# Optimization experiments

Hardware: AMD Instinct MI355X
Metric: run time of the kernel (lower is better)

## Reference

```python
import jax, jax.numpy as jnp
import numpy as np

RCUT = 6.0
EPS = 1e-6
NUM_BASIS = 8
P = 6  # PolynomialSmooth envelope power
N_NODES = 100000
N_EDGES = 3200000
N_GRAPHS = 16

# 27 periodic image shifts: all integer combos of [-1,0,1]^3
_PERIODIC = jnp.asarray(
    np.stack(np.meshgrid(*([[-1, 0, 1]] * 3), indexing='ij'), -1).reshape(27, 3).astype(np.float32)
)


def _sh_lmax2(u):
    """e3nn spherical harmonics, lmax=2, normalize=True, normalization='component'.
    u: [E,3] unit vectors -> [E,9]."""
    x, y, z = u[..., 0], u[..., 1], u[..., 2]
    s3 = jnp.sqrt(jnp.asarray(3.0, u.dtype))
    s5 = jnp.sqrt(jnp.asarray(5.0, u.dtype))
    s15 = jnp.sqrt(jnp.asarray(15.0, u.dtype))
    return jnp.stack([
        jnp.ones_like(x),                      # l=0
        s3 * x, s3 * y, s3 * z,                # l=1
        s15 * x * z,                           # l=2
        s15 * x * y,
        s5 * (y * y - 0.5 * (x * x + z * z)),
        s15 * y * z,
        0.5 * s15 * (z * z - x * x),
    ], axis=-1)


def _bessel(lengths):
    # lengths: [E,1] -> [E,NUM_BASIS]
    k = jnp.arange(1, NUM_BASIS + 1, dtype=lengths.dtype) * jnp.pi / RCUT
    safe = jnp.clip(lengths, EPS, RCUT)
    return jnp.sin(safe * k) / (2.0 * safe)


def _poly_smooth(lengths):
    # standard polynomial envelope (DimeNet-style), zero at r=rcut
    x = jnp.clip(lengths / RCUT, 0.0, 1.0)
    c1 = (P + 1) * (P + 2) / 2.0
    c2 = float(P * (P + 2))
    c3 = P * (P + 1) / 2.0
    xp = x ** P
    return 1.0 - c1 * xp + c2 * xp * x - c3 * xp * x * x


def setup_inputs() -> dict:
    key = jax.random.key(0)
    k1, k2, k3, k4, k5 = jax.random.split(key, 5)
    pos = jax.random.normal(k1, (N_NODES, 3), dtype=jnp.float32) * 5.0
    cells = jax.random.normal(k2, (N_GRAPHS, 3, 3), dtype=jnp.float32)
    edge_index = jax.random.randint(k3, (2, N_EDGES), 0, N_NODES)
    periodic_index = jax.random.randint(k4, (N_EDGES,), 0, 27)
    batch = jnp.sort(jax.random.randint(k5, (N_NODES,), 0, N_GRAPHS))
    return {"pos": pos, "cells": cells, "edge_index": edge_index,
            "periodic_index": periodic_index, "batch": batch}


def reference(pos, cells, edge_index, periodic_index, batch):
    node_src, node_dst = edge_index[0], edge_index[1]
    vectors = pos[node_dst] - pos[node_src]                     # [E,3]
    shifts = _PERIODIC[periodic_index]                          # [E,3]
    src_cells = cells[batch[node_src]]                          # [E,3,3]
    vectors = vectors - jnp.einsum('eij,ei->ej', src_cells, shifts)
    vectors = -vectors                                          # dst == 'atom'
    lengths = jnp.linalg.norm(vectors, axis=-1, keepdims=True)  # [E,1]
    unit = vectors / jnp.maximum(lengths, EPS)                  # normalize=True
    attr = _sh_lmax2(unit)                                      # [E,9]
    basis = _bessel(lengths)                                    # [E,8]
    cutoff = _poly_smooth(lengths)                              # [E,1]
    basis_weight = basis * cutoff                               # [E,8]
    # pack (length, sh attr, smooth, basis_weight) -> [E,19]
    return jnp.concatenate([lengths, attr, cutoff, basis_weight], axis=-1)
```

## Files before the change

kernel.cpp:

```cpp
#include <hip/hip_runtime.h>

#define BLOCK 256

typedef float vf4 __attribute__((ext_vector_type(4)));

extern "C" __global__ void __launch_bounds__(BLOCK) pack_pos_batch(
    const float* __restrict__ pos,
    const int*  __restrict__ batch,
    vf4* __restrict__ pos4,
    int N)
{
    const int i = blockIdx.x * BLOCK + threadIdx.x;
    if (i < N) {
        vf4 v;
        v.x = pos[3 * i + 0];
        v.y = pos[3 * i + 1];
        v.z = pos[3 * i + 2];
        v.w = __int_as_float(batch[i]);
        pos4[i] = v;
    }
}

template <bool PACKED>
__global__ void __launch_bounds__(BLOCK) edge_encoding_kernel(
    const float* __restrict__ pos,
    const vf4*   __restrict__ pos4,
    const float* __restrict__ cells,
    const int*   __restrict__ eidx,
    const int*   __restrict__ pidx,
    const int*   __restrict__ batch,
    float* __restrict__ out,
    int E)
{
    __shared__ float s_cells[144];
    __shared__ __align__(16) float s_out[BLOCK * 19];

    const int tid = threadIdx.x;
    if (tid < 144) s_cells[tid] = cells[tid];
    __syncthreads();

    const int base = blockIdx.x * BLOCK;
    const int e = base + tid;

    float row[19];
    if (e < E) {
        const int src = __builtin_nontemporal_load(eidx + e);
        const int dst = __builtin_nontemporal_load(eidx + E + e);
        const int p   = __builtin_nontemporal_load(pidx + e);

        float sx, sy, sz, dx, dy, dz;
        int g;
        if (PACKED) {
            const vf4 ps = pos4[src];
            const vf4 pd = pos4[dst];
            sx = ps.x; sy = ps.y; sz = ps.z;
            dx = pd.x; dy = pd.y; dz = pd.z;
            g  = __float_as_int(ps.w);
        } else {
            sx = pos[3*src+0]; sy = pos[3*src+1]; sz = pos[3*src+2];
            dx = pos[3*dst+0]; dy = pos[3*dst+1]; dz = pos[3*dst+2];
            g  = batch[src];
        }

        const float f0 = (float)(p / 9 - 1);
        const float f1 = (float)((p / 3) % 3 - 1);
        const float f2 = (float)(p % 3 - 1);

        const float* C = s_cells + g * 9;
        const float tx = C[0]*f0 + C[3]*f1 + C[6]*f2;
        const float ty = C[1]*f0 + C[4]*f1 + C[7]*f2;
        const float tz = C[2]*f0 + C[5]*f1 + C[8]*f2;

        const float vx = sx - dx + tx;
        const float vy = sy - dy + ty;
        const float vz = sz - dz + tz;

        const float len  = sqrtf(vx*vx + vy*vy + vz*vz);
        const float invl = 1.0f / fmaxf(len, 1e-6f);
        const float x = vx * invl, y = vy * invl, z = vz * invl;

        const float s3  = 1.7320508075688772f;
        const float s5  = 2.2360679774997896f;
        const float s15 = 3.872983346207417f;

        row[0] = len;
        row[1] = 1.0f;
        row[2] = s3 * x;
        row[3] = s3 * y;
        row[4] = s3 * z;
        row[5] = s15 * x * z;
        row[6] = s15 * x * y;
        row[7] = s5  * (y*y - 0.5f*(x*x + z*z));
        row[8] = s15 * y * z;
        row[9] = 0.5f * s15 * (z*z - x*x);

        const float xc = fminf(len * (1.0f/6.0f), 1.0f);
        const float x3 = xc * xc * xc;
        const float x6 = x3 * x3;
        const float cut = fmaf(x6, fmaf(xc, fmaf(-21.0f, xc, 48.0f), -28.0f), 1.0f);
        row[10] = cut;

        const float safe = fminf(fmaxf(len, 1e-6f), 6.0f);
        const float a = safe * 0.5235987755982988f;
        const float sa = __sinf(a);
        const float ca = __cosf(a);
        const float w = cut / (2.0f * safe);
        const float two_ca = 2.0f * ca;
        float s_prev = 0.0f, s_cur = sa;
        row[11] = s_cur * w;
        #pragma unroll
        for (int n = 2; n <= 8; ++n) {
            const float s_next = two_ca * s_cur - s_prev;
            s_prev = s_cur;
            s_cur  = s_next;
            row[10 + n] = s_cur * w;
        }
    } else {
        #pragma unroll
        for (int j = 0; j < 19; ++j) row[j] = 0.0f;
    }

    #pragma unroll
    for (int j = 0; j < 19; ++j) s_out[tid * 19 + j] = row[j];
    __syncthreads();

    const int nvalid  = min(BLOCK, E - base);
    const int nfloats = nvalid * 19;
    float* gout = out + (size_t)base * 19;
    const int n4 = nfloats >> 2;
    const vf4* s4 = reinterpret_cast<const vf4*>(s_out);
    vf4* g4 = reinterpret_cast<vf4*>(gout);
    for (int i = tid; i < n4; i += BLOCK)
        __builtin_nontemporal_store(s4[i], g4 + i);
    for (int i = (n4 << 2) + tid; i < nfloats; i += BLOCK)
        __builtin_nontemporal_store(s_out[i], gout + i);
}

extern "C" void kernel_launch(void* const* d_in, const int* in_sizes, int n_in,
                              void* d_out, int out_size, void* d_ws, size_t ws_size,
                              hipStream_t stream) {
    const float* pos   = (const float*)d_in[0];
    const float* cells = (const float*)d_in[1];
    const int*   eidx  = (const int*)d_in[2];
    const int*   pidx  = (const int*)d_in[3];
    const int*   batch = (const int*)d_in[4];
    float* out = (float*)d_out;

    const int E = in_sizes[3];
    const int N = in_sizes[4];
    const int grid = (E + BLOCK - 1) / BLOCK;

    if (d_ws != nullptr && ws_size >= (size_t)N * sizeof(vf4)) {
        vf4* pos4 = (vf4*)d_ws;
        const int pgrid = (N + BLOCK - 1) / BLOCK;
        pack_pos_batch<<<pgrid, BLOCK, 0, stream>>>(pos, batch, pos4, N);
        edge_encoding_kernel<true><<<grid, BLOCK, 0, stream>>>(
            pos, pos4, cells, eidx, pidx, batch, out, E);
    } else {
        edge_encoding_kernel<false><<<grid, BLOCK, 0, stream>>>(
            pos, nullptr, cells, eidx, pidx, batch, out, E);
    }
}
```

Measured before the change: 294.6 us.

## Convert edge kernel to persistent grid with software-pipelined index loads and gathers

The edge kernel now runs on a fixed grid of 2048 persistent blocks that loop over tiles. Each iteration prefetches indices two tiles ahead and position gathers one tile ahead, and writes the previous tile's staged output while the current tile is computed. The goal is to hide gather latency and overlap output stores with compute. The two divisions are also replaced with fast hardware reciprocals. The cost is higher register pressure and extra barriers per tile, and the reciprocal is slightly less accurate.

```diff
diff --git a/kernel.cpp b/kernel.cpp
--- a/kernel.cpp
+++ b/kernel.cpp
@@ -1,6 +1,7 @@
 #include <hip/hip_runtime.h>
 
 #define BLOCK 256
+#define NBLOCKS 2048
 
 typedef float vf4 __attribute__((ext_vector_type(4)));
 
@@ -37,103 +38,149 @@
 
     const int tid = threadIdx.x;
     if (tid < 144) s_cells[tid] = cells[tid];
+
+    const int ntiles = (E + BLOCK - 1) / BLOCK;
+    const int nb = gridDim.x;
+
+    const float s3  = 1.7320508075688772f;
+    const float s5  = 2.2360679774997896f;
+    const float s15 = 3.872983346207417f;
+
+    int src1, dst1, p0, p1;
+    vf4 g_ps, g_pd;
+
+    auto load_idx = [&](int tt, int& s, int& d, int& p) {
+        if (tt < ntiles) {
+            int e = tt * BLOCK + tid;
+            e = min(e, E - 1);
+            s = __builtin_nontemporal_load(eidx + e);
+            d = __builtin_nontemporal_load(eidx + E + e);
+            p = __builtin_nontemporal_load(pidx + e);
+        } else { s = 0; d = 0; p = 13; }
+    };
+    auto gather = [&](int s, int d, vf4& a, vf4& b) {
+        if (PACKED) {
+            a = pos4[s];
+            b = pos4[d];
+        } else {
+            a.x = pos[3*s+0]; a.y = pos[3*s+1]; a.z = pos[3*s+2];
+            a.w = __int_as_float(batch[s]);
+            b.x = pos[3*d+0]; b.y = pos[3*d+1]; b.z = pos[3*d+2];
+            b.w = 0.0f;
+        }
+    };
+
+    int t = blockIdx.x;
+    {
+        int s0, d0;
+        load_idx(t, s0, d0, p0);
+        gather(s0, d0, g_ps, g_pd);
+        load_idx(t + nb, src1, dst1, p1);
+    }
     __syncthreads();
 
-    const int base = blockIdx.x * BLOCK;
-    const int e = base + tid;
-
-    float row[19];
-    if (e < E) {
-        const int src = __builtin_nontemporal_load(eidx + e);
-        const int dst = __builtin_nontemporal_load(eidx + E + e);
-        const int p   = __builtin_nontemporal_load(pidx + e);
-
-        float sx, sy, sz, dx, dy, dz;
-        int g;
-        if (PACKED) {
-            const vf4 ps = pos4[src];
-            const vf4 pd = pos4[dst];
-            sx = ps.x; sy = ps.y; sz = ps.z;
-            dx = pd.x; dy = pd.y; dz = pd.z;
-            g  = __float_as_int(ps.w);
-        } else {
-            sx = pos[3*src+0]; sy = pos[3*src+1]; sz = pos[3*src+2];
-            dx = pos[3*dst+0]; dy = pos[3*dst+1]; dz = pos[3*dst+2];
-            g  = batch[src];
+    int tprev = -1;
+    for (; t < ntiles; t += nb) {
+        int src2, dst2, p2;
+        load_idx(t + 2 * nb, src2, dst2, p2);
+        vf4 n_ps, n_pd;
+        gather(src1, dst1, n_ps, n_pd);
+
+        if (tprev >= 0) {
+            const int nvalid  = min(BLOCK, E - tprev * BLOCK);
+            const int nfloats = nvalid * 19;
+            float* gout = out + (size_t)tprev * BLOCK * 19;
+            const int n4 = nfloats >> 2;
+            const vf4* s4 = reinterpret_cast<const vf4*>(s_out);
+            vf4* g4 = reinterpret_cast<vf4*>(gout);
+            for (int i = tid; i < n4; i += BLOCK)
+                __builtin_nontemporal_store(s4[i], g4 + i);
+            for (int i = (n4 << 2) + tid; i < nfloats; i += BLOCK)
+                __builtin_nontemporal_store(s_out[i], gout + i);
         }
 
-        const float f0 = (float)(p / 9 - 1);
-        const float f1 = (float)((p / 3) % 3 - 1);
-        const float f2 = (float)(p % 3 - 1);
-
-        const float* C = s_cells + g * 9;
-        const float tx = C[0]*f0 + C[3]*f1 + C[6]*f2;
-        const float ty = C[1]*f0 + C[4]*f1 + C[7]*f2;
-        const float tz = C[2]*f0 + C[5]*f1 + C[8]*f2;
-
-        const float vx = sx - dx + tx;
-        const float vy = sy - dy + ty;
-        const float vz = sz - dz + tz;
-
-        const float len  = sqrtf(vx*vx + vy*vy + vz*vz);
-        const float invl = 1.0f / fmaxf(len, 1e-6f);
-        const float x = vx * invl, y = vy * invl, z = vz * invl;
-
-        const float s3  = 1.7320508075688772f;
-        const float s5  = 2.2360679774997896f;
-        const float s15 = 3.872983346207417f;
-
-        row[0] = len;
-        row[1] = 1.0f;
-        row[2] = s3 * x;
-        row[3] = s3 * y;
-        row[4] = s3 * z;
-        row[5] = s15 * x * z;
-        row[6] = s15 * x * y;
-        row[7] = s5  * (y*y - 0.5f*(x*x + z*z));
-        row[8] = s15 * y * z;
-        row[9] = 0.5f * s15 * (z*z - x*x);
-
-        const float xc = fminf(len * (1.0f/6.0f), 1.0f);
-        const float x3 = xc * xc * xc;
-        const float x6 = x3 * x3;
-        const float cut = fmaf(x6, fmaf(xc, fmaf(-21.0f, xc, 48.0f), -28.0f), 1.0f);
-        row[10] = cut;
-
-        const float safe = fminf(fmaxf(len, 1e-6f), 6.0f);
-        const float a = safe * 0.5235987755982988f;
-        const float sa = __sinf(a);
-        const float ca = __cosf(a);
-        const float w = cut / (2.0f * safe);
-        const float two_ca = 2.0f * ca;
-        float s_prev = 0.0f, s_cur = sa;
-        row[11] = s_cur * w;
+        float row[19];
+        {
+            const float sx = g_ps.x, sy = g_ps.y, sz = g_ps.z;
+            const float dx = g_pd.x, dy = g_pd.y, dz = g_pd.z;
+            const int   g  = PACKED ? __float_as_int(g_ps.w)
+                                    : __float_as_int(g_ps.w);
+            const int   p  = p0;
+
+            const float f0 = (float)(p / 9 - 1);
+            const float f1 = (float)((p / 3) % 3 - 1);
+            const float f2 = (float)(p % 3 - 1);
+
+            const float* C = s_cells + g * 9;
+            const float tx = C[0]*f0 + C[3]*f1 + C[6]*f2;
+            const float ty = C[1]*f0 + C[4]*f1 + C[7]*f2;
+            const float tz = C[2]*f0 + C[5]*f1 + C[8]*f2;
+
+            const float vx = sx - dx + tx;
+            const float vy = sy - dy + ty;
+            const float vz = sz - dz + tz;
+
+            const float len  = sqrtf(vx*vx + vy*vy + vz*vz);
+            const float invl = __builtin_amdgcn_rcpf(fmaxf(len, 1e-6f));
+            const float x = vx * invl, y = vy * invl, z = vz * invl;
+
+            row[0] = len;
+            row[1] = 1.0f;
+            row[2] = s3 * x;
+            row[3] = s3 * y;
+            row[4] = s3 * z;
+            row[5] = s15 * x * z;
+            row[6] = s15 * x * y;
+            row[7] = s5  * (y*y - 0.5f*(x*x + z*z));
+            row[8] = s15 * y * z;
+            row[9] = 0.5f * s15 * (z*z - x*x);
+
+            const float xc = fminf(len * (1.0f/6.0f), 1.0f);
+            const float x3 = xc * xc * xc;
+            const float x6 = x3 * x3;
+            const float cut = fmaf(x6, fmaf(xc, fmaf(-21.0f, xc, 48.0f), -28.0f), 1.0f);
+            row[10] = cut;
+
+            const float safe = fminf(fmaxf(len, 1e-6f), 6.0f);
+            const float a = safe * 0.5235987755982988f;
+            const float sa = __sinf(a);
+            const float ca = __cosf(a);
+            const float w = cut * 0.5f * __builtin_amdgcn_rcpf(safe);
+            const float two_ca = 2.0f * ca;
+            float s_prev = 0.0f, s_cur = sa;
+            row[11] = s_cur * w;
+            #pragma unroll
+            for (int n = 2; n <= 8; ++n) {
+                const float s_next = two_ca * s_cur - s_prev;
+                s_prev = s_cur;
+                s_cur  = s_next;
+                row[10 + n] = s_cur * w;
+            }
+        }
+
+        __syncthreads();
         #pragma unroll
-        for (int n = 2; n <= 8; ++n) {
-            const float s_next = two_ca * s_cur - s_prev;
-            s_prev = s_cur;
-            s_cur  = s_next;
-            row[10 + n] = s_cur * w;
-        }
-    } else {
-        #pragma unroll
-        for (int j = 0; j < 19; ++j) row[j] = 0.0f;
-    }
-
-    #pragma unroll
-    for (int j = 0; j < 19; ++j) s_out[tid * 19 + j] = row[j];
-    __syncthreads();
-
-    const int nvalid  = min(BLOCK, E - base);
-    const int nfloats = nvalid * 19;
-    float* gout = out + (size_t)base * 19;
-    const int n4 = nfloats >> 2;
-    const vf4* s4 = reinterpret_cast<const vf4*>(s_out);
-    vf4* g4 = reinterpret_cast<vf4*>(gout);
-    for (int i = tid; i < n4; i += BLOCK)
-        __builtin_nontemporal_store(s4[i], g4 + i);
-    for (int i = (n4 << 2) + tid; i < nfloats; i += BLOCK)
-        __builtin_nontemporal_store(s_out[i], gout + i);
+        for (int j = 0; j < 19; ++j) s_out[tid * 19 + j] = row[j];
+        __syncthreads();
+
+        g_ps = n_ps; g_pd = n_pd;
+        p0 = p1;
+        src1 = src2; dst1 = dst2; p1 = p2;
+        tprev = t;
+    }
+
+    if (tprev >= 0) {
+        const int nvalid  = min(BLOCK, E - tprev * BLOCK);
+        const int nfloats = nvalid * 19;
+        float* gout = out + (size_t)tprev * BLOCK * 19;
+        const int n4 = nfloats >> 2;
+        const vf4* s4 = reinterpret_cast<const vf4*>(s_out);
+        vf4* g4 = reinterpret_cast<vf4*>(gout);
+        for (int i = tid; i < n4; i += BLOCK)
+            __builtin_nontemporal_store(s4[i], g4 + i);
+        for (int i = (n4 << 2) + tid; i < nfloats; i += BLOCK)
+            __builtin_nontemporal_store(s_out[i], gout + i);
+    }
 }
 
 extern "C" void kernel_launch(void* const* d_in, const int* in_sizes, int n_in,
@@ -148,7 +195,8 @@
 
     const int E = in_sizes[3];
     const int N = in_sizes[4];
-    const int grid = (E + BLOCK - 1) / BLOCK;
+    const int ntiles = (E + BLOCK - 1) / BLOCK;
+    const int grid = ntiles < NBLOCKS ? ntiles : NBLOCKS;
 
     if (d_ws != nullptr && ws_size >= (size_t)N * sizeof(vf4)) {
         vf4* pos4 = (vf4*)d_ws;
```

Measured after the change: 311.5 us. +5.7%, slower.

## Process four edges per thread with vector loads and direct vector stores

Applied to the files above, without the earlier changes.

Each thread now handles four consecutive edges. It loads the src, dst and periodic indices as int4 vectors and writes its 76 output floats straight to global memory as 19 float4 nontemporal stores, so the LDS staging buffer and its second barrier are gone. The 16x27 periodic translation table is precomputed into shared memory per block, and the divides are replaced with hardware reciprocal approximations. The per-thread buffer raises register pressure and may reduce occupancy. Each lane's stores are contiguous, so across a wavefront they are strided rather than fully coalesced.

```diff
diff --git a/kernel.cpp b/kernel.cpp
--- a/kernel.cpp
+++ b/kernel.cpp
@@ -1,8 +1,10 @@
 #include <hip/hip_runtime.h>
 
 #define BLOCK 256
+#define EPT 4
 
 typedef float vf4 __attribute__((ext_vector_type(4)));
+typedef int   vi4 __attribute__((ext_vector_type(4)));
 
 extern "C" __global__ void __launch_bounds__(BLOCK) pack_pos_batch(
     const float* __restrict__ pos,
@@ -32,57 +34,83 @@
     float* __restrict__ out,
     int E)
 {
-    __shared__ float s_cells[144];
-    __shared__ __align__(16) float s_out[BLOCK * 19];
+    __shared__ vf4 s_t[16 * 27];
 
     const int tid = threadIdx.x;
-    if (tid < 144) s_cells[tid] = cells[tid];
-    __syncthreads();
-
-    const int base = blockIdx.x * BLOCK;
-    const int e = base + tid;
-
-    float row[19];
-    if (e < E) {
-        const int src = __builtin_nontemporal_load(eidx + e);
-        const int dst = __builtin_nontemporal_load(eidx + E + e);
-        const int p   = __builtin_nontemporal_load(pidx + e);
-
-        float sx, sy, sz, dx, dy, dz;
-        int g;
-        if (PACKED) {
-            const vf4 ps = pos4[src];
-            const vf4 pd = pos4[dst];
-            sx = ps.x; sy = ps.y; sz = ps.z;
-            dx = pd.x; dy = pd.y; dz = pd.z;
-            g  = __float_as_int(ps.w);
-        } else {
-            sx = pos[3*src+0]; sy = pos[3*src+1]; sz = pos[3*src+2];
-            dx = pos[3*dst+0]; dy = pos[3*dst+1]; dz = pos[3*dst+2];
-            g  = batch[src];
-        }
-
+    for (int c = tid; c < 16 * 27; c += BLOCK) {
+        const int g = c / 27, p = c % 27;
         const float f0 = (float)(p / 9 - 1);
         const float f1 = (float)((p / 3) % 3 - 1);
         const float f2 = (float)(p % 3 - 1);
+        const float* C = cells + g * 9;
+        vf4 t;
+        t.x = C[0]*f0 + C[3]*f1 + C[6]*f2;
+        t.y = C[1]*f0 + C[4]*f1 + C[7]*f2;
+        t.z = C[2]*f0 + C[5]*f1 + C[8]*f2;
+        t.w = 0.0f;
+        s_t[c] = t;
+    }
+    __syncthreads();
 
-        const float* C = s_cells + g * 9;
-        const float tx = C[0]*f0 + C[3]*f1 + C[6]*f2;
-        const float ty = C[1]*f0 + C[4]*f1 + C[7]*f2;
-        const float tz = C[2]*f0 + C[5]*f1 + C[8]*f2;
+    const long long gtid = (long long)blockIdx.x * BLOCK + tid;
+    const long long e0   = gtid * EPT;
+    if (e0 >= E) return;
 
-        const float vx = sx - dx + tx;
-        const float vy = sy - dy + ty;
-        const float vz = sz - dz + tz;
+    const bool full = (e0 + EPT <= (long long)E);
+    const bool evec = ((E & 3) == 0);
+
+    int src[EPT], dst[EPT], pp[EPT];
+    if (full && evec) {
+        const vi4 s = __builtin_nontemporal_load((const vi4*)(eidx + e0));
+        const vi4 d = __builtin_nontemporal_load((const vi4*)(eidx + E + e0));
+        const vi4 q = __builtin_nontemporal_load((const vi4*)(pidx + e0));
+        src[0]=s.x; src[1]=s.y; src[2]=s.z; src[3]=s.w;
+        dst[0]=d.x; dst[1]=d.y; dst[2]=d.z; dst[3]=d.w;
+        pp[0]=q.x;  pp[1]=q.y;  pp[2]=q.z;  pp[3]=q.w;
+    } else {
+        #pragma unroll
+        for (int k = 0; k < EPT; ++k) {
+            long long e = e0 + k; if (e >= E) e = E - 1;
+            src[k] = eidx[e];
+            dst[k] = eidx[E + e];
+            pp[k]  = pidx[e];
+        }
+    }
+
+    vf4 ps[EPT], pd[EPT];
+    #pragma unroll
+    for (int k = 0; k < EPT; ++k) {
+        if (PACKED) {
+            ps[k] = pos4[src[k]];
+            pd[k] = pos4[dst[k]];
+        } else {
+            const int s = src[k], d = dst[k];
+            ps[k].x = pos[3*s+0]; ps[k].y = pos[3*s+1]; ps[k].z = pos[3*s+2];
+            ps[k].w = __int_as_float(batch[s]);
+            pd[k].x = pos[3*d+0]; pd[k].y = pos[3*d+1]; pd[k].z = pos[3*d+2];
+            pd[k].w = 0.0f;
+        }
+    }
+
+    const float s3  = 1.7320508075688772f;
+    const float s5  = 2.2360679774997896f;
+    const float s15 = 3.872983346207417f;
+
+    float buf[EPT * 19];
+    #pragma unroll
+    for (int k = 0; k < EPT; ++k) {
+        const int g = __float_as_int(ps[k].w);
+        const vf4 t = s_t[g * 27 + pp[k]];
+
+        const float vx = ps[k].x - pd[k].x + t.x;
+        const float vy = ps[k].y - pd[k].y + t.y;
+        const float vz = ps[k].z - pd[k].z + t.z;
 
         const float len  = sqrtf(vx*vx + vy*vy + vz*vz);
-        const float invl = 1.0f / fmaxf(len, 1e-6f);
+        const float invl = __builtin_amdgcn_rcpf(fmaxf(len, 1e-6f));
         const float x = vx * invl, y = vy * invl, z = vz * invl;
 
-        const float s3  = 1.7320508075688772f;
-        const float s5  = 2.2360679774997896f;
-        const float s15 = 3.872983346207417f;
-
+        float* row = buf + k * 19;
         row[0] = len;
         row[1] = 1.0f;
         row[2] = s3 * x;
@@ -104,7 +132,7 @@
         const float a = safe * 0.5235987755982988f;
         const float sa = __sinf(a);
         const float ca = __cosf(a);
-        const float w = cut / (2.0f * safe);
+        const float w = cut * 0.5f * __builtin_amdgcn_rcpf(safe);
         const float two_ca = 2.0f * ca;
         float s_prev = 0.0f, s_cur = sa;
         row[11] = s_cur * w;
@@ -115,25 +143,22 @@
             s_cur  = s_next;
             row[10 + n] = s_cur * w;
         }
-    } else {
-        #pragma unroll
-        for (int j = 0; j < 19; ++j) row[j] = 0.0f;
     }
 
-    #pragma unroll
-    for (int j = 0; j < 19; ++j) s_out[tid * 19 + j] = row[j];
-    __syncthreads();
-
-    const int nvalid  = min(BLOCK, E - base);
-    const int nfloats = nvalid * 19;
-    float* gout = out + (size_t)base * 19;
-    const int n4 = nfloats >> 2;
-    const vf4* s4 = reinterpret_cast<const vf4*>(s_out);
-    vf4* g4 = reinterpret_cast<vf4*>(gout);
-    for (int i = tid; i < n4; i += BLOCK)
-        __builtin_nontemporal_store(s4[i], g4 + i);
-    for (int i = (n4 << 2) + tid; i < nfloats; i += BLOCK)
-        __builtin_nontemporal_store(s_out[i], gout + i);
+    float* gout = out + e0 * 19;
+    if (full) {
+        #pragma unroll
+        for (int i = 0; i < 19; ++i) {
+            vf4 v;
+            v.x = buf[4*i+0]; v.y = buf[4*i+1]; v.z = buf[4*i+2]; v.w = buf[4*i+3];
+            __builtin_nontemporal_store(v, (vf4*)gout + i);
+        }
+    } else {
+        const int nvalid = (int)(E - e0);
+        for (int k = 0; k < nvalid; ++k)
+            for (int j = 0; j < 19; ++j)
+                gout[k*19 + j] = buf[k*19 + j];
+    }
 }
 
 extern "C" void kernel_launch(void* const* d_in, const int* in_sizes, int n_in,
@@ -148,7 +173,7 @@
 
     const int E = in_sizes[3];
     const int N = in_sizes[4];
-    const int grid = (E + BLOCK - 1) / BLOCK;
+    const int grid = (int)(((long long)E + BLOCK * EPT - 1) / (BLOCK * EPT));
 
     if (d_ws != nullptr && ws_size >= (size_t)N * sizeof(vf4)) {
         vf4* pos4 = (vf4*)d_ws;
```

Measured after the change: 805.7 us. 2.73x slower.

## Process four edges per thread with batched gathers and precomputed shift table

Applied to the files above, without the earlier changes.

Each thread now handles four edges, issuing all index loads and then all position gathers before computing, so more memory requests are in flight per thread. Cell-times-shift translations for all 16 graphs and 27 images are precomputed into shared memory, and the divides are replaced with hardware reciprocal approximations. The shared staging buffer is reused per sub-tile, which adds extra barriers and raises register pressure, and launches four times fewer blocks.

```diff
diff --git a/kernel.cpp b/kernel.cpp
--- a/kernel.cpp
+++ b/kernel.cpp
@@ -1,6 +1,8 @@
 #include <hip/hip_runtime.h>
 
 #define BLOCK 256
+#define EPT 4
+#define TILE (BLOCK * EPT)
 
 typedef float vf4 __attribute__((ext_vector_type(4)));
 
@@ -32,108 +34,124 @@
     float* __restrict__ out,
     int E)
 {
-    __shared__ float s_cells[144];
+    __shared__ vf4 s_t[16 * 27];
     __shared__ __align__(16) float s_out[BLOCK * 19];
 
     const int tid = threadIdx.x;
-    if (tid < 144) s_cells[tid] = cells[tid];
-    __syncthreads();
-
-    const int base = blockIdx.x * BLOCK;
-    const int e = base + tid;
-
-    float row[19];
-    if (e < E) {
-        const int src = __builtin_nontemporal_load(eidx + e);
-        const int dst = __builtin_nontemporal_load(eidx + E + e);
-        const int p   = __builtin_nontemporal_load(pidx + e);
-
-        float sx, sy, sz, dx, dy, dz;
-        int g;
-        if (PACKED) {
-            const vf4 ps = pos4[src];
-            const vf4 pd = pos4[dst];
-            sx = ps.x; sy = ps.y; sz = ps.z;
-            dx = pd.x; dy = pd.y; dz = pd.z;
-            g  = __float_as_int(ps.w);
-        } else {
-            sx = pos[3*src+0]; sy = pos[3*src+1]; sz = pos[3*src+2];
-            dx = pos[3*dst+0]; dy = pos[3*dst+1]; dz = pos[3*dst+2];
-            g  = batch[src];
-        }
-
+    for (int c = tid; c < 16 * 27; c += BLOCK) {
+        const int g = c / 27, p = c % 27;
         const float f0 = (float)(p / 9 - 1);
         const float f1 = (float)((p / 3) % 3 - 1);
         const float f2 = (float)(p % 3 - 1);
+        const float* C = cells + g * 9;
+        vf4 t;
+        t.x = C[0]*f0 + C[3]*f1 + C[6]*f2;
+        t.y = C[1]*f0 + C[4]*f1 + C[7]*f2;
+        t.z = C[2]*f0 + C[5]*f1 + C[8]*f2;
+        t.w = 0.0f;
+        s_t[c] = t;
+    }
+    __syncthreads();
 
-        const float* C = s_cells + g * 9;
-        const float tx = C[0]*f0 + C[3]*f1 + C[6]*f2;
-        const float ty = C[1]*f0 + C[4]*f1 + C[7]*f2;
-        const float tz = C[2]*f0 + C[5]*f1 + C[8]*f2;
+    const long long b0 = (long long)blockIdx.x * TILE;
 
-        const float vx = sx - dx + tx;
-        const float vy = sy - dy + ty;
-        const float vz = sz - dz + tz;
-
-        const float len  = sqrtf(vx*vx + vy*vy + vz*vz);
-        const float invl = 1.0f / fmaxf(len, 1e-6f);
-        const float x = vx * invl, y = vy * invl, z = vz * invl;
-
-        const float s3  = 1.7320508075688772f;
-        const float s5  = 2.2360679774997896f;
-        const float s15 = 3.872983346207417f;
-
-        row[0] = len;
-        row[1] = 1.0f;
-        row[2] = s3 * x;
-        row[3] = s3 * y;
-        row[4] = s3 * z;
-        row[5] = s15 * x * z;
-        row[6] = s15 * x * y;
-        row[7] = s5  * (y*y - 0.5f*(x*x + z*z));
-        row[8] = s15 * y * z;
-        row[9] = 0.5f * s15 * (z*z - x*x);
-
-        const float xc = fminf(len * (1.0f/6.0f), 1.0f);
-        const float x3 = xc * xc * xc;
-        const float x6 = x3 * x3;
-        const float cut = fmaf(x6, fmaf(xc, fmaf(-21.0f, xc, 48.0f), -28.0f), 1.0f);
-        row[10] = cut;
-
-        const float safe = fminf(fmaxf(len, 1e-6f), 6.0f);
-        const float a = safe * 0.5235987755982988f;
-        const float sa = __sinf(a);
-        const float ca = __cosf(a);
-        const float w = cut / (2.0f * safe);
-        const float two_ca = 2.0f * ca;
-        float s_prev = 0.0f, s_cur = sa;
-        row[11] = s_cur * w;
-        #pragma unroll
-        for (int n = 2; n <= 8; ++n) {
-            const float s_next = two_ca * s_cur - s_prev;
-            s_prev = s_cur;
-            s_cur  = s_next;
-            row[10 + n] = s_cur * w;
+    int src[EPT], dst[EPT], pp[EPT];
+    #pragma unroll
+    for (int r = 0; r < EPT; ++r) {
+        long long e = b0 + (long long)r * BLOCK + tid;
+        if (e >= E) e = E - 1;
+        src[r] = __builtin_nontemporal_load(eidx + e);
+        dst[r] = __builtin_nontemporal_load(eidx + E + e);
+        pp[r]  = __builtin_nontemporal_load(pidx + e);
+    }
+    vf4 ps[EPT], pd[EPT];
+    #pragma unroll
+    for (int r = 0; r < EPT; ++r) {
+        if (PACKED) {
+            ps[r] = pos4[src[r]];
+            pd[r] = pos4[dst[r]];
+        } else {
+            const int s = src[r], d = dst[r];
+            ps[r].x = pos[3*s+0]; ps[r].y = pos[3*s+1]; ps[r].z = pos[3*s+2];
+            ps[r].w = __int_as_float(batch[s]);
+            pd[r].x = pos[3*d+0]; pd[r].y = pos[3*d+1]; pd[r].z = pos[3*d+2];
+            pd[r].w = 0.0f;
         }
-    } else {
-        #pragma unroll
-        for (int j = 0; j < 19; ++j) row[j] = 0.0f;
     }
 
+    const float s3  = 1.7320508075688772f;
+    const float s5  = 2.2360679774997896f;
+    const float s15 = 3.872983346207417f;
+
     #pragma unroll
-    for (int j = 0; j < 19; ++j) s_out[tid * 19 + j] = row[j];
-    __syncthreads();
+    for (int c = 0; c < EPT; ++c) {
+        float row[19];
+        {
+            const int g = __float_as_int(ps[c].w);
+            const vf4 t = s_t[g * 27 + pp[c]];
 
-    const int nvalid  = min(BLOCK, E - base);
-    const int nfloats = nvalid * 19;
-    float* gout = out + (size_t)base * 19;
-    const int n4 = nfloats >> 2;
-    const vf4* s4 = reinterpret_cast<const vf4*>(s_out);
-    vf4* g4 = reinterpret_cast<vf4*>(gout);
-    for (int i = tid; i < n4; i += BLOCK)
-        __builtin_nontemporal_store(s4[i], g4 + i);
-    for (int i = (n4 << 2) + tid; i < nfloats; i += BLOCK)
-        __builtin_nontemporal_store(s_out[i], gout + i);
+            const float vx = ps[c].x - pd[c].x + t.x;
+            const float vy = ps[c].y - pd[c].y + t.y;
+            const float vz = ps[c].z - pd[c].z + t.z;
+
+            const float len  = sqrtf(vx*vx + vy*vy + vz*vz);
+            const float invl = __builtin_amdgcn_rcpf(fmaxf(len, 1e-6f));
+            const float x = vx * invl, y = vy * invl, z = vz * invl;
+
+            row[0] = len;
+            row[1] = 1.0f;
+            row[2] = s3 * x;
+            row[3] = s3 * y;
+            row[4] = s3 * z;
+            row[5] = s15 * x * z;
+            row[6] = s15 * x * y;
+            row[7] = s5  * (y*y - 0.5f*(x*x + z*z));
+            row[8] = s15 * y * z;
+            row[9] = 0.5f * s15 * (z*z - x*x);
+
+            const float xc = fminf(len * (1.0f/6.0f), 1.0f);
+            const float x3 = xc * xc * xc;
+            const float x6 = x3 * x3;
+            const float cut = fmaf(x6, fmaf(xc, fmaf(-21.0f, xc, 48.0f), -28.0f), 1.0f);
+            row[10] = cut;
+
+            const float safe = fminf(fmaxf(len, 1e-6f), 6.0f);
+            const float a = safe * 0.5235987755982988f;
+            const float sa = __sinf(a);
+            const float ca = __cosf(a);
+            const float w = cut * 0.5f * __builtin_amdgcn_rcpf(safe);
+            const float two_ca = 2.0f * ca;
+            float s_prev = 0.0f, s_cur = sa;
+            row[11] = s_cur * w;
+            #pragma unroll
+            for (int n = 2; n <= 8; ++n) {
+                const float s_next = two_ca * s_cur - s_prev;
+                s_prev = s_cur;
+                s_cur  = s_next;
+                row[10 + n] = s_cur * w;
+            }
+        }
+
+        if (c > 0) __syncthreads();
+
+        #pragma unroll
+        for (int j = 0; j < 19; ++j) s_out[tid * 19 + j] = row[j];
+        __syncthreads();
+
+        const long long base_e = b0 + (long long)c * BLOCK;
+        if (base_e < E) {
+            const int nvalid  = (int)min((long long)BLOCK, (long long)E - base_e);
+            const int nfloats = nvalid * 19;
+            float* gout = out + base_e * 19;
+            const int n4 = nfloats >> 2;
+            const vf4* s4 = reinterpret_cast<const vf4*>(s_out);
+            vf4* g4 = reinterpret_cast<vf4*>(gout);
+            for (int i = tid; i < n4; i += BLOCK)
+                __builtin_nontemporal_store(s4[i], g4 + i);
+            for (int i = (n4 << 2) + tid; i < nfloats; i += BLOCK)
+                __builtin_nontemporal_store(s_out[i], gout + i);
+        }
+    }
 }
 
 extern "C" void kernel_launch(void* const* d_in, const int* in_sizes, int n_in,
@@ -148,7 +166,7 @@
 
     const int E = in_sizes[3];
     const int N = in_sizes[4];
-    const int grid = (E + BLOCK - 1) / BLOCK;
+    const int grid = (int)(((long long)E + TILE - 1) / TILE);
 
     if (d_ws != nullptr && ws_size >= (size_t)N * sizeof(vf4)) {
         vf4* pos4 = (vf4*)d_ws;
```

Measured after the change: 316.5 us. 7.4% more time.
